# Kernel optimization log

Hardware: AMD Instinct MI355X
Metric: run time of the kernel (lower is better)

## Reference

```python
import jax, jax.numpy as jnp
import numpy as np

N_NODES = 50000
NEG_SLOPE = 0.2  # PyG GATConv default leaky_relu slope


def gat_conv(x, src, dst, W, a_src, a_dst, b):
    """One PyG-style GATConv (concat heads, add_self_loops already applied).
    x: [N, F_in]; W: [H*C, F_in]; a_src/a_dst: [H, C]; b: [H*C]."""
    N = x.shape[0]
    H, C = a_src.shape
    h = (x @ W.T).reshape(N, H, C)                       # [N,H,C]
    alpha_src = jnp.einsum('nhc,hc->nh', h, a_src)       # [N,H]
    alpha_dst = jnp.einsum('nhc,hc->nh', h, a_dst)       # [N,H]
    e = alpha_src[src] + alpha_dst[dst]                  # [E,H]
    e = jax.nn.leaky_relu(e, NEG_SLOPE)
    # segment softmax over incoming edges of each dst node, per head
    m = jax.ops.segment_max(e, dst, num_segments=N)      # [N,H]
    w = jnp.exp(e - m[dst])                              # [E,H]
    s = jax.ops.segment_sum(w, dst, num_segments=N)      # [N,H]
    alpha = w / (s[dst] + 1e-16)                         # [E,H]
    msg = alpha[:, :, None] * h[src]                     # [E,H,C]
    out = jax.ops.segment_sum(msg, dst, num_segments=N)  # [N,H,C]
    return out.reshape(N, H * C) + b


def setup_inputs() -> dict:
    key = jax.random.key(0)
    ks = jax.random.split(key, 8)
    N, E, F_in, H, C, L = N_NODES, 800000, 128, 4, 32, 3
    x = jax.random.normal(ks[0], (N, F_in), dtype=jnp.float32)
    edge_index = jax.random.randint(ks[1], (2, E), 0, N, dtype=jnp.int32)
    Ws = jax.random.normal(ks[2], (L, H * C, F_in), dtype=jnp.float32) * 0.1
    att_src = jax.random.normal(ks[3], (L, H, C), dtype=jnp.float32) * 0.1
    att_dst = jax.random.normal(ks[4], (L, H, C), dtype=jnp.float32) * 0.1
    conv_bias = jnp.zeros((L, H * C), dtype=jnp.float32)
    Wf = jax.random.normal(ks[5], (32, H * C), dtype=jnp.float32) * 0.1
    bf = jnp.zeros((32,), dtype=jnp.float32)
    return {"x": x, "Ws": Ws, "att_src": att_src, "att_dst": att_dst,
            "conv_bias": conv_bias, "Wf": Wf, "bf": bf, "edge_index": edge_index}


def reference(x, Ws, att_src, att_dst, conv_bias, Wf, bf, edge_index):
    N = x.shape[0]
    # PyG GATConv add_self_loops=True (default): append i->i for every node
    loop = jnp.arange(N, dtype=edge_index.dtype)
    src = jnp.concatenate([edge_index[0], loop])
    dst = jnp.concatenate([edge_index[1], loop])
    for l in range(Ws.shape[0]):
        x = gat_conv(x, src, dst, Ws[l], att_src[l], att_dst[l], conv_bias[l])
        x = jax.nn.relu(x)
        # F.dropout(p=0.1, training=False) is identity in eval mode
    return x @ Wf.T + bf
```

## Files before the change

kernel.cpp:

```cpp
#include <hip/hip_runtime.h>
#include <hip/hip_bf16.h>
#include <math.h>

#define N_NODES 50000
#define NE      800000
#define ETOT    (NE + N_NODES)
#define F       128
#define NHEAD   4
#define NEG     0.2f

#define SCAN_B 256
#define NBLK   ((N_NODES + SCAN_B - 1) / SCAN_B)

typedef __attribute__((ext_vector_type(8))) short bf16x8;
typedef __attribute__((ext_vector_type(4))) float f32x4;
typedef _Float16 f16x8 __attribute__((ext_vector_type(8)));


__global__ void k_deg(const int* __restrict__ ei, int* __restrict__ deg,
                      int* __restrict__ rank) {
    int i = blockIdx.x * blockDim.x + threadIdx.x;
    if (i < ETOT) {
        int d = (i < NE) ? ei[NE + i] : (i - NE);
        rank[i] = atomicAdd(&deg[d], 1);
    }
}

__global__ void k_scan1(const int* __restrict__ deg, int* __restrict__ bsum) {
    __shared__ int sm[SCAN_B];
    int i = blockIdx.x * SCAN_B + threadIdx.x;
    sm[threadIdx.x] = (i < N_NODES) ? deg[i] : 0;
    __syncthreads();
    for (int s = SCAN_B / 2; s > 0; s >>= 1) {
        if (threadIdx.x < s) sm[threadIdx.x] += sm[threadIdx.x + s];
        __syncthreads();
    }
    if (threadIdx.x == 0) bsum[blockIdx.x] = sm[0];
}

__global__ void k_scan2(int* __restrict__ bsum) {
    __shared__ int sm[SCAN_B];
    int t = threadIdx.x;
    int v = (t < NBLK) ? bsum[t] : 0;
    sm[t] = v; __syncthreads();
    for (int s = 1; s < SCAN_B; s <<= 1) {
        int a = (t >= s) ? sm[t - s] : 0;
        __syncthreads();
        sm[t] += a;
        __syncthreads();
    }
    if (t < NBLK) bsum[t] = sm[t] - v;
}

__global__ void k_scan3(const int* __restrict__ deg, const int* __restrict__ bsum,
                        int* __restrict__ rowptr) {
    __shared__ int sm[SCAN_B];
    int t = threadIdx.x;
    int i = blockIdx.x * SCAN_B + t;
    int v = (i < N_NODES) ? deg[i] : 0;
    sm[t] = v; __syncthreads();
    for (int s = 1; s < SCAN_B; s <<= 1) {
        int a = (t >= s) ? sm[t - s] : 0;
        __syncthreads();
        sm[t] += a;
        __syncthreads();
    }
    int excl = sm[t] - v + bsum[blockIdx.x];
    if (i < N_NODES) rowptr[i] = excl;
    if (i == N_NODES - 1) rowptr[N_NODES] = excl + v;
}

__global__ void k_fill(const int* __restrict__ ei, const int* __restrict__ rowptr,
                       const int* __restrict__ rank, int* __restrict__ col) {
    int i = blockIdx.x * blockDim.x + threadIdx.x;
    if (i < ETOT) {
        int s, d;
        if (i < NE) { s = ei[i]; d = ei[NE + i]; }
        else        { s = i - NE; d = s; }
        col[rowptr[d] + rank[i]] = s;
    }
}


__device__ __forceinline__ unsigned short f2bf(float x) {
    unsigned int u = __float_as_uint(x);
    u += 0x7FFFu + ((u >> 16) & 1u);
    return (unsigned short)(u >> 16);
}
__device__ __forceinline__ float bf2f(unsigned short h) {
    return __uint_as_float(((unsigned int)h) << 16);
}
__device__ __forceinline__ void cvt8(float4 a, float4 b, bf16x8* hi, bf16x8* lo) {
    float f[8] = {a.x, a.y, a.z, a.w, b.x, b.y, b.z, b.w};
    bf16x8 h, l;
#pragma unroll
    for (int j = 0; j < 8; j++) {
        unsigned short hu = f2bf(f[j]);
        h[j] = (short)hu;
        l[j] = (short)f2bf(f[j] - bf2f(hu));
    }
    *hi = h; *lo = l;
}
__device__ __forceinline__ void cvt8h(float4 a, float4 b, f16x8* hi, f16x8* lo) {
    float f[8] = {a.x, a.y, a.z, a.w, b.x, b.y, b.z, b.w};
    f16x8 h, l;
#pragma unroll
    for (int j = 0; j < 8; j++) {
        _Float16 hh = (_Float16)f[j];
        h[j] = hh;
        l[j] = (_Float16)(f[j] - (float)hh);
    }
    *hi = h; *lo = l;
}

__device__ __forceinline__ int lds_unit(int m, int q) {
    return 4 * m + (q ^ ((m >> 1) & 3));
}

#define GM 64


__global__ __launch_bounds__(256) void k_gemm(const float* __restrict__ X,
                                              const float* __restrict__ W,
                                              const float* __restrict__ a_s,
                                              const float* __restrict__ a_d,
                                              _Float16* __restrict__ hout,
                                              float* __restrict__ asrc,
                                              float* __restrict__ adst) {
    __shared__ short Ah[256 * 8], Al[256 * 8];
    __shared__ short Bh[512 * 8], Bl[512 * 8];
    int tid = threadIdx.x;
    int bm = blockIdx.x * GM;

    int am = tid >> 2, aq = tid & 3;
    int xunit = ((am >> 4) << 6) + lds_unit(am & 15, aq);
    int wj = tid >> 2, wq = tid & 3;
    int wunit = ((wj >> 4) << 6) + lds_unit(wj & 15, wq);

    int lane = tid & 63, wv = tid >> 6;
    int fm = lane & 15, fq = lane >> 4;
    int a_unit = (wv << 6) + lds_unit(fm, fq);
    int b_unit0 = lds_unit(fm, fq);

    f32x4 acc[8];
#pragma unroll
    for (int nt = 0; nt < 8; nt++) acc[nt] = (f32x4){0.f, 0.f, 0.f, 0.f};

    float4 xp0, xp1, wp0, wp1, wp2, wp3;
    int gr = bm + am;
    bool xok = (gr < N_NODES);
    const float* xrow = X + (size_t)gr * F + aq * 8;
    const float* wrow1 = W + (size_t)wj * F + wq * 8;
    const float* wrow2 = W + (size_t)(wj + 64) * F + wq * 8;
    float4 z4 = make_float4(0.f, 0.f, 0.f, 0.f);

    auto load_tile = [&](int k0) {
        xp0 = xok ? *(const float4*)(xrow + k0)     : z4;
        xp1 = xok ? *(const float4*)(xrow + k0 + 4) : z4;
        wp0 = *(const float4*)(wrow1 + k0);
        wp1 = *(const float4*)(wrow1 + k0 + 4);
        wp2 = *(const float4*)(wrow2 + k0);
        wp3 = *(const float4*)(wrow2 + k0 + 4);
    };
    auto store_tile = [&]() {
        bf16x8 hi, lo;
        cvt8(xp0, xp1, &hi, &lo);
        *(bf16x8*)&Ah[xunit * 8] = hi;  *(bf16x8*)&Al[xunit * 8] = lo;
        cvt8(wp0, wp1, &hi, &lo);
        *(bf16x8*)&Bh[wunit * 8] = hi;  *(bf16x8*)&Bl[wunit * 8] = lo;
        cvt8(wp2, wp3, &hi, &lo);
        *(bf16x8*)&Bh[(wunit + 256) * 8] = hi;  *(bf16x8*)&Bl[(wunit + 256) * 8] = lo;
    };

    load_tile(0);
    store_tile();
    __syncthreads();

#pragma unroll
    for (int t = 0; t < 4; t++) {
        if (t < 3) load_tile((t + 1) * 32);
        bf16x8 ah = *(bf16x8*)&Ah[a_unit * 8];
        bf16x8 al = *(bf16x8*)&Al[a_unit * 8];
#pragma unroll
        for (int nt = 0; nt < 8; nt++) {
            int bu = ((nt << 6) + b_unit0) * 8;
            bf16x8 bh = *(bf16x8*)&Bh[bu];
            bf16x8 bl = *(bf16x8*)&Bl[bu];
            acc[nt] = __builtin_amdgcn_mfma_f32_16x16x32_bf16(ah, bh, acc[nt], 0, 0, 0);
            acc[nt] = __builtin_amdgcn_mfma_f32_16x16x32_bf16(ah, bl, acc[nt], 0, 0, 0);
            acc[nt] = __builtin_amdgcn_mfma_f32_16x16x32_bf16(al, bh, acc[nt], 0, 0, 0);
        }
        __syncthreads();
        if (t < 3) { store_tile(); __syncthreads(); }
    }

    float as_v[8], ad_v[8];
#pragma unroll
    for (int nt = 0; nt < 8; nt++) {
        as_v[nt] = a_s[nt * 16 + fm];
        ad_v[nt] = a_d[nt * 16 + fm];
    }
#pragma unroll
    for (int r = 0; r < 4; r++) {
        int n = bm + wv * 16 + fq * 4 + r;
        bool ok = (n < N_NODES);
        if (ok) {
#pragma unroll
            for (int nt = 0; nt < 8; nt++)
                hout[(size_t)n * F + nt * 16 + fm] = (_Float16)acc[nt][r];
        }
        float ps[4], pd[4];
#pragma unroll
        for (int hh = 0; hh < 4; hh++) {
            ps[hh] = acc[2 * hh][r] * as_v[2 * hh] + acc[2 * hh + 1][r] * as_v[2 * hh + 1];
            pd[hh] = acc[2 * hh][r] * ad_v[2 * hh] + acc[2 * hh + 1][r] * ad_v[2 * hh + 1];
        }
#pragma unroll
        for (int s = 1; s < 16; s <<= 1) {
#pragma unroll
            for (int hh = 0; hh < 4; hh++) {
                ps[hh] += __shfl_xor(ps[hh], s);
                pd[hh] += __shfl_xor(pd[hh], s);
            }
        }
        if (ok && fm == 0) {
            *(float4*)&asrc[n * 4] = make_float4(ps[0], ps[1], ps[2], ps[3]);
            *(float4*)&adst[n * 4] = make_float4(pd[0], pd[1], pd[2], pd[3]);
        }
    }
}


__global__ __launch_bounds__(256) void k_gemm16(const _Float16* __restrict__ X,
                                                const float* __restrict__ W,
                                                const float* __restrict__ a_s,
                                                const float* __restrict__ a_d,
                                                _Float16* __restrict__ hout,
                                                float* __restrict__ asrc,
                                                float* __restrict__ adst) {
    __shared__ _Float16 Ahf[256 * 8];
    __shared__ _Float16 Bhf[512 * 8], Blf[512 * 8];
    int tid = threadIdx.x;
    int bm = blockIdx.x * GM;

    int am = tid >> 2, aq = tid & 3;
    int xunit = ((am >> 4) << 6) + lds_unit(am & 15, aq);
    int wj = tid >> 2, wq = tid & 3;
    int wunit = ((wj >> 4) << 6) + lds_unit(wj & 15, wq);

    int lane = tid & 63, wv = tid >> 6;
    int fm = lane & 15, fq = lane >> 4;
    int a_unit = (wv << 6) + lds_unit(fm, fq);
    int b_unit0 = lds_unit(fm, fq);

    f32x4 acc[8];
#pragma unroll
    for (int nt = 0; nt < 8; nt++) acc[nt] = (f32x4){0.f, 0.f, 0.f, 0.f};

    f16x8 xp;
    float4 wp0, wp1, wp2, wp3;
    int gr = bm + am;
    bool xok = (gr < N_NODES);
    const _Float16* xrow = X + (size_t)gr * F + aq * 8;
    const float* wrow1 = W + (size_t)wj * F + wq * 8;
    const float* wrow2 = W + (size_t)(wj + 64) * F + wq * 8;

    auto load_tile = [&](int k0) {
        f16x8 zz = {0, 0, 0, 0, 0, 0, 0, 0};
        xp = xok ? *(const f16x8*)(xrow + k0) : zz;
        wp0 = *(const float4*)(wrow1 + k0);
        wp1 = *(const float4*)(wrow1 + k0 + 4);
        wp2 = *(const float4*)(wrow2 + k0);
        wp3 = *(const float4*)(wrow2 + k0 + 4);
    };
    auto store_tile = [&]() {
        *(f16x8*)&Ahf[xunit * 8] = xp;
        f16x8 hi, lo;
        cvt8h(wp0, wp1, &hi, &lo);
        *(f16x8*)&Bhf[wunit * 8] = hi;  *(f16x8*)&Blf[wunit * 8] = lo;
        cvt8h(wp2, wp3, &hi, &lo);
        *(f16x8*)&Bhf[(wunit + 256) * 8] = hi;  *(f16x8*)&Blf[(wunit + 256) * 8] = lo;
    };

    load_tile(0);
    store_tile();
    __syncthreads();

#pragma unroll
    for (int t = 0; t < 4; t++) {
        if (t < 3) load_tile((t + 1) * 32);
        f16x8 ah = *(f16x8*)&Ahf[a_unit * 8];
#pragma unroll
        for (int nt = 0; nt < 8; nt++) {
            int bu = ((nt << 6) + b_unit0) * 8;
            f16x8 bh = *(f16x8*)&Bhf[bu];
            f16x8 bl = *(f16x8*)&Blf[bu];
            acc[nt] = __builtin_amdgcn_mfma_f32_16x16x32_f16(ah, bh, acc[nt], 0, 0, 0);
            acc[nt] = __builtin_amdgcn_mfma_f32_16x16x32_f16(ah, bl, acc[nt], 0, 0, 0);
        }
        __syncthreads();
        if (t < 3) { store_tile(); __syncthreads(); }
    }

    float as_v[8], ad_v[8];
#pragma unroll
    for (int nt = 0; nt < 8; nt++) {
        as_v[nt] = a_s[nt * 16 + fm];
        ad_v[nt] = a_d[nt * 16 + fm];
    }
#pragma unroll
    for (int r = 0; r < 4; r++) {
        int n = bm + wv * 16 + fq * 4 + r;
        bool ok = (n < N_NODES);
        if (ok) {
#pragma unroll
            for (int nt = 0; nt < 8; nt++)
                hout[(size_t)n * F + nt * 16 + fm] = (_Float16)acc[nt][r];
        }
        float ps[4], pd[4];
#pragma unroll
        for (int hh = 0; hh < 4; hh++) {
            ps[hh] = acc[2 * hh][r] * as_v[2 * hh] + acc[2 * hh + 1][r] * as_v[2 * hh + 1];
            pd[hh] = acc[2 * hh][r] * ad_v[2 * hh] + acc[2 * hh + 1][r] * ad_v[2 * hh + 1];
        }
#pragma unroll
        for (int s = 1; s < 16; s <<= 1) {
#pragma unroll
            for (int hh = 0; hh < 4; hh++) {
                ps[hh] += __shfl_xor(ps[hh], s);
                pd[hh] += __shfl_xor(pd[hh], s);
            }
        }
        if (ok && fm == 0) {
            *(float4*)&asrc[n * 4] = make_float4(ps[0], ps[1], ps[2], ps[3]);
            *(float4*)&adst[n * 4] = make_float4(pd[0], pd[1], pd[2], pd[3]);
        }
    }
}


#define EPAD 68

__global__ __launch_bounds__(256) void k_aggr(const _Float16* __restrict__ h,
                                              const float* __restrict__ asrc,
                                              const float* __restrict__ adst,
                                              const int* __restrict__ rowptr,
                                              const int* __restrict__ col,
                                              const float* __restrict__ bias,
                                              _Float16* __restrict__ xout) {
    __shared__ int   scol[4][64];
    __shared__ float swT[4][4 * EPAD];
    int wave = threadIdx.x >> 6;
    int lane = threadIdx.x & 63;
    int n = blockIdx.x * 4 + wave;
    if (n >= N_NODES) return;
    int wl = lane & 15;
    int he = lane >> 4;
    int hc = wl >> 2;
    int beg = rowptr[n], end = rowptr[n + 1];
    float4 ad4 = *(const float4*)&adst[n * 4];

    float s_run = 0.f;
    float acc[8];
#pragma unroll
    for (int j = 0; j < 8; j++) acc[j] = 0.f;

    for (int base = beg; base < end; base += 64) {
        int cnt = end - base; if (cnt > 64) cnt = 64;
        int sidx = 0;
        float4 w4 = make_float4(0.f, 0.f, 0.f, 0.f);
        if (lane < cnt) {
            sidx = col[base + lane];
            float4 av = *(const float4*)&asrc[sidx * 4];
            float ex = av.x + ad4.x, ey = av.y + ad4.y,
                  ez = av.z + ad4.z, ew = av.w + ad4.w;
            ex = (ex > 0.f) ? ex : NEG * ex;
            ey = (ey > 0.f) ? ey : NEG * ey;
            ez = (ez > 0.f) ? ez : NEG * ez;
            ew = (ew > 0.f) ? ew : NEG * ew;
            w4.x = __expf(ex); w4.y = __expf(ey);
            w4.z = __expf(ez); w4.w = __expf(ew);
        }
        scol[wave][lane] = sidx;
        swT[wave][0 * EPAD + lane] = w4.x;
        swT[wave][1 * EPAD + lane] = w4.y;
        swT[wave][2 * EPAD + lane] = w4.z;
        swT[wave][3 * EPAD + lane] = w4.w;
        __builtin_amdgcn_sched_barrier(0);
        float4 wv4 = *(float4*)&swT[wave][he * EPAD + wl * 4];
        float S = (wv4.x + wv4.y) + (wv4.z + wv4.w);
#pragma unroll
        for (int s = 1; s < 16; s <<= 1) S += __shfl_xor(S, s);
        s_run += S;
        __builtin_amdgcn_sched_barrier(0);
#pragma unroll 2
        for (int p = 0; p < cnt; p += 4) {
            int ep = p + he;
            int s = scol[wave][ep];
            float wgt = swT[wave][hc * EPAD + ep];
            f16x8 hv = *(const f16x8*)&h[(size_t)s * F + wl * 8];
#pragma unroll
            for (int j = 0; j < 8; j++)
                acc[j] = fmaf(wgt, (float)hv[j], acc[j]);
        }
        __builtin_amdgcn_sched_barrier(0);
    }

#pragma unroll
    for (int j = 0; j < 8; j++) {
        acc[j] += __shfl_xor(acc[j], 16);
        acc[j] += __shfl_xor(acc[j], 32);
    }
    float sv = __shfl(s_run, hc * 16);
    float inv = 1.f / (sv + 1e-16f);
    float4 b0 = *(const float4*)&bias[wl * 8];
    float4 b1 = *(const float4*)&bias[wl * 8 + 4];
    float bb[8] = {b0.x, b0.y, b0.z, b0.w, b1.x, b1.y, b1.z, b1.w};
    if (he == 0) {
        f16x8 st;
#pragma unroll
        for (int j = 0; j < 8; j++)
            st[j] = (_Float16)fmaxf(fmaf(acc[j], inv, bb[j]), 0.f);
        *(f16x8*)&xout[(size_t)n * F + wl * 8] = st;
    }
}


#define FCB 128

__global__ __launch_bounds__(256) void k_fc(const _Float16* __restrict__ X,
                                            const float* __restrict__ Wf,
                                            const float* __restrict__ bf,
                                            float* __restrict__ out) {
    __shared__ float WsT[128 * 36];
    __shared__ float XsT[32 * 132];
    int tid = threadIdx.x;
    int bm = blockIdx.x * FCB;

#pragma unroll
    for (int u = 0; u < 16; u++) {
        int idx = tid + 256 * u;
        int o = idx & 31, k = idx >> 5;
        WsT[k * 36 + o] = Wf[o * 128 + k];
    }

    int tx = tid & 7;
    int ty = tid >> 3;
    float acc[4][4];
#pragma unroll
    for (int i = 0; i < 4; i++)
#pragma unroll
        for (int j = 0; j < 4; j++) acc[i][j] = 0.f;

    for (int k0 = 0; k0 < 128; k0 += 32) {
        __syncthreads();
#pragma unroll
        for (int u = 0; u < 2; u++) {
            int idx = tid + 256 * u;
            int nn = idx & 127, c = idx >> 7;
            int gn = bm + nn;
            f16x8 v = {0, 0, 0, 0, 0, 0, 0, 0};
            if (gn < N_NODES) v = *(const f16x8*)&X[(size_t)gn * F + k0 + c * 8];
#pragma unroll
            for (int j = 0; j < 8; j++)
                XsT[(c * 8 + j) * 132 + nn] = (float)v[j];
        }
        __syncthreads();

#pragma unroll
        for (int kk = 0; kk < 32; kk++) {
            float4 xv = *(float4*)&XsT[kk * 132 + ty * 4];
            float4 wv = *(float4*)&WsT[(k0 + kk) * 36 + tx * 4];
            float xs[4] = {xv.x, xv.y, xv.z, xv.w};
            float ws[4] = {wv.x, wv.y, wv.z, wv.w};
#pragma unroll
            for (int i = 0; i < 4; i++)
#pragma unroll
                for (int j = 0; j < 4; j++)
                    acc[i][j] = fmaf(xs[i], ws[j], acc[i][j]);
        }
    }

    float4 bv = *(const float4*)&bf[tx * 4];
#pragma unroll
    for (int i = 0; i < 4; i++) {
        int n = bm + ty * 4 + i;
        if (n < N_NODES) {
            float4 o4 = make_float4(acc[i][0] + bv.x, acc[i][1] + bv.y,
                                    acc[i][2] + bv.z, acc[i][3] + bv.w);
            *(float4*)&out[n * 32 + tx * 4] = o4;
        }
    }
}


extern "C" void kernel_launch(void* const* d_in, const int* in_sizes, int n_in,
                              void* d_out, int out_size, void* d_ws, size_t ws_size,
                              hipStream_t stream) {
    const float* x      = (const float*)d_in[0];
    const float* Ws     = (const float*)d_in[1];
    const float* a_src  = (const float*)d_in[2];
    const float* a_dst  = (const float*)d_in[3];
    const float* cbias  = (const float*)d_in[4];
    const float* Wf     = (const float*)d_in[5];
    const float* bf     = (const float*)d_in[6];
    const int*   ei     = (const int*)d_in[7];
    float* out = (float*)d_out;

    char* p = (char*)d_ws;
    auto carve = [&](size_t bytes) {
        char* r = p;
        p += (bytes + 255) & ~(size_t)255;
        return r;
    };
    _Float16* xA   = (_Float16*)carve((size_t)N_NODES * F * 2);
    _Float16* xB   = (_Float16*)carve((size_t)N_NODES * F * 2);
    _Float16* xC   = (_Float16*)carve((size_t)N_NODES * F * 2);
    _Float16* hbuf = (_Float16*)carve((size_t)N_NODES * F * 2);
    float* asrc = (float*)carve((size_t)N_NODES * NHEAD * 4);
    float* adst = (float*)carve((size_t)N_NODES * NHEAD * 4);
    int* deg    = (int*)carve((size_t)N_NODES * 4);
    int* rowptr = (int*)carve((size_t)(N_NODES + 1) * 4);
    int* rank   = (int*)carve((size_t)ETOT * 4);
    int* bsum   = (int*)carve((size_t)SCAN_B * 4);
    int* col    = (int*)carve((size_t)ETOT * 4);

    hipMemsetAsync(deg, 0, (size_t)N_NODES * 4, stream);
    k_deg<<<(ETOT + 255) / 256, 256, 0, stream>>>(ei, deg, rank);
    k_scan1<<<NBLK, SCAN_B, 0, stream>>>(deg, bsum);
    k_scan2<<<1, SCAN_B, 0, stream>>>(bsum);
    k_scan3<<<NBLK, SCAN_B, 0, stream>>>(deg, bsum, rowptr);
    k_fill<<<(ETOT + 255) / 256, 256, 0, stream>>>(ei, rowptr, rank, col);

    int gaggr = (N_NODES + 3) / 4;
    int ggemm = (N_NODES + GM - 1) / GM;

    k_gemm<<<ggemm, 256, 0, stream>>>(x, Ws, a_src, a_dst, hbuf, asrc, adst);
    k_aggr<<<gaggr, 256, 0, stream>>>(hbuf, asrc, adst, rowptr, col, cbias, xA);

    k_gemm16<<<ggemm, 256, 0, stream>>>(xA, Ws + (size_t)F * F, a_src + F, a_dst + F,
                                        hbuf, asrc, adst);
    k_aggr<<<gaggr, 256, 0, stream>>>(hbuf, asrc, adst, rowptr, col, cbias + F, xB);

    k_gemm16<<<ggemm, 256, 0, stream>>>(xB, Ws + (size_t)2 * F * F, a_src + 2 * F,
                                        a_dst + 2 * F, hbuf, asrc, adst);
    k_aggr<<<gaggr, 256, 0, stream>>>(hbuf, asrc, adst, rowptr, col, cbias + 2 * F, xC);

    k_fc<<<(N_NODES + FCB - 1) / FCB, 256, 0, stream>>>(xC, Wf, bf, out);
}
```

Measured before the change: 323.9 us.

## Pre-split weights to fp16 hi/lo and stage GEMM tiles via global_load_lds double buffering

A new prep kernel converts the fp32 layer weights once per call into fp16 high and low parts, so the GEMMs no longer redo the split in every block. Weight tiles, and the fp16 activations in later layers, are now copied straight into LDS with global_load_lds into double buffers, which removes one barrier per K step. The first-layer GEMM moves from a bf16 three-way split to an fp16 three-way split. This adds one small kernel launch and extra workspace, drops the LDS swizzle (so bank conflicts may appear), and changes precision characteristics for layer one.

```diff
diff --git a/kernel.cpp b/kernel.cpp
--- a/kernel.cpp
+++ b/kernel.cpp
@@ -12,9 +12,14 @@
 #define SCAN_B 256
 #define NBLK   ((N_NODES + SCAN_B - 1) / SCAN_B)
 
-typedef __attribute__((ext_vector_type(8))) short bf16x8;
 typedef __attribute__((ext_vector_type(4))) float f32x4;
 typedef _Float16 f16x8 __attribute__((ext_vector_type(8)));
+
+__device__ __forceinline__ void gld16(const void* g, void* l) {
+    __builtin_amdgcn_global_load_lds(
+        (const __attribute__((address_space(1))) unsigned int*)g,
+        (__attribute__((address_space(3))) unsigned int*)l, 16, 0, 0);
+}
 
 
 __global__ void k_deg(const int* __restrict__ ei, int* __restrict__ deg,
@@ -82,118 +87,22 @@
 }
 
 
-__device__ __forceinline__ unsigned short f2bf(float x) {
-    unsigned int u = __float_as_uint(x);
-    u += 0x7FFFu + ((u >> 16) & 1u);
-    return (unsigned short)(u >> 16);
-}
-__device__ __forceinline__ float bf2f(unsigned short h) {
-    return __uint_as_float(((unsigned int)h) << 16);
-}
-__device__ __forceinline__ void cvt8(float4 a, float4 b, bf16x8* hi, bf16x8* lo) {
-    float f[8] = {a.x, a.y, a.z, a.w, b.x, b.y, b.z, b.w};
-    bf16x8 h, l;
-#pragma unroll
-    for (int j = 0; j < 8; j++) {
-        unsigned short hu = f2bf(f[j]);
-        h[j] = (short)hu;
-        l[j] = (short)f2bf(f[j] - bf2f(hu));
-    }
-    *hi = h; *lo = l;
-}
-__device__ __forceinline__ void cvt8h(float4 a, float4 b, f16x8* hi, f16x8* lo) {
-    float f[8] = {a.x, a.y, a.z, a.w, b.x, b.y, b.z, b.w};
-    f16x8 h, l;
-#pragma unroll
-    for (int j = 0; j < 8; j++) {
-        _Float16 hh = (_Float16)f[j];
-        h[j] = hh;
-        l[j] = (_Float16)(f[j] - (float)hh);
-    }
-    *hi = h; *lo = l;
-}
-
-__device__ __forceinline__ int lds_unit(int m, int q) {
-    return 4 * m + (q ^ ((m >> 1) & 3));
-}
+__global__ void k_prep(const float* __restrict__ Ws, _Float16* __restrict__ Wh,
+                       _Float16* __restrict__ Wl) {
+    int i = blockIdx.x * blockDim.x + threadIdx.x;
+    float w = Ws[i];
+    _Float16 h = (_Float16)w;
+    Wh[i] = h;
+    Wl[i] = (_Float16)(w - (float)h);
+}
+
 
 #define GM 64
 
-
-__global__ __launch_bounds__(256) void k_gemm(const float* __restrict__ X,
-                                              const float* __restrict__ W,
-                                              const float* __restrict__ a_s,
-                                              const float* __restrict__ a_d,
-                                              _Float16* __restrict__ hout,
-                                              float* __restrict__ asrc,
-                                              float* __restrict__ adst) {
-    __shared__ short Ah[256 * 8], Al[256 * 8];
-    __shared__ short Bh[512 * 8], Bl[512 * 8];
-    int tid = threadIdx.x;
-    int bm = blockIdx.x * GM;
-
-    int am = tid >> 2, aq = tid & 3;
-    int xunit = ((am >> 4) << 6) + lds_unit(am & 15, aq);
-    int wj = tid >> 2, wq = tid & 3;
-    int wunit = ((wj >> 4) << 6) + lds_unit(wj & 15, wq);
-
-    int lane = tid & 63, wv = tid >> 6;
-    int fm = lane & 15, fq = lane >> 4;
-    int a_unit = (wv << 6) + lds_unit(fm, fq);
-    int b_unit0 = lds_unit(fm, fq);
-
-    f32x4 acc[8];
-#pragma unroll
-    for (int nt = 0; nt < 8; nt++) acc[nt] = (f32x4){0.f, 0.f, 0.f, 0.f};
-
-    float4 xp0, xp1, wp0, wp1, wp2, wp3;
-    int gr = bm + am;
-    bool xok = (gr < N_NODES);
-    const float* xrow = X + (size_t)gr * F + aq * 8;
-    const float* wrow1 = W + (size_t)wj * F + wq * 8;
-    const float* wrow2 = W + (size_t)(wj + 64) * F + wq * 8;
-    float4 z4 = make_float4(0.f, 0.f, 0.f, 0.f);
-
-    auto load_tile = [&](int k0) {
-        xp0 = xok ? *(const float4*)(xrow + k0)     : z4;
-        xp1 = xok ? *(const float4*)(xrow + k0 + 4) : z4;
-        wp0 = *(const float4*)(wrow1 + k0);
-        wp1 = *(const float4*)(wrow1 + k0 + 4);
-        wp2 = *(const float4*)(wrow2 + k0);
-        wp3 = *(const float4*)(wrow2 + k0 + 4);
-    };
-    auto store_tile = [&]() {
-        bf16x8 hi, lo;
-        cvt8(xp0, xp1, &hi, &lo);
-        *(bf16x8*)&Ah[xunit * 8] = hi;  *(bf16x8*)&Al[xunit * 8] = lo;
-        cvt8(wp0, wp1, &hi, &lo);
-        *(bf16x8*)&Bh[wunit * 8] = hi;  *(bf16x8*)&Bl[wunit * 8] = lo;
-        cvt8(wp2, wp3, &hi, &lo);
-        *(bf16x8*)&Bh[(wunit + 256) * 8] = hi;  *(bf16x8*)&Bl[(wunit + 256) * 8] = lo;
-    };
-
-    load_tile(0);
-    store_tile();
-    __syncthreads();
-
-#pragma unroll
-    for (int t = 0; t < 4; t++) {
-        if (t < 3) load_tile((t + 1) * 32);
-        bf16x8 ah = *(bf16x8*)&Ah[a_unit * 8];
-        bf16x8 al = *(bf16x8*)&Al[a_unit * 8];
-#pragma unroll
-        for (int nt = 0; nt < 8; nt++) {
-            int bu = ((nt << 6) + b_unit0) * 8;
-            bf16x8 bh = *(bf16x8*)&Bh[bu];
-            bf16x8 bl = *(bf16x8*)&Bl[bu];
-            acc[nt] = __builtin_amdgcn_mfma_f32_16x16x32_bf16(ah, bh, acc[nt], 0, 0, 0);
-            acc[nt] = __builtin_amdgcn_mfma_f32_16x16x32_bf16(ah, bl, acc[nt], 0, 0, 0);
-            acc[nt] = __builtin_amdgcn_mfma_f32_16x16x32_bf16(al, bh, acc[nt], 0, 0, 0);
-        }
-        __syncthreads();
-        if (t < 3) { store_tile(); __syncthreads(); }
-    }
-
+__device__ __forceinline__ void gemm_epilogue(
+        f32x4* acc, const float* a_s, const float* a_d,
+        _Float16* hout, float* asrc, float* adst,
+        int bm, int wv, int fm, int fq) {
     float as_v[8], ad_v[8];
 #pragma unroll
     for (int nt = 0; nt < 8; nt++) {
@@ -231,111 +140,144 @@
 }
 
 
-__global__ __launch_bounds__(256) void k_gemm16(const _Float16* __restrict__ X,
-                                                const float* __restrict__ W,
+__global__ __launch_bounds__(256) void k_gemm32(const float* __restrict__ X,
+                                                const _Float16* __restrict__ Wh,
+                                                const _Float16* __restrict__ Wl,
                                                 const float* __restrict__ a_s,
                                                 const float* __restrict__ a_d,
                                                 _Float16* __restrict__ hout,
                                                 float* __restrict__ asrc,
                                                 float* __restrict__ adst) {
-    __shared__ _Float16 Ahf[256 * 8];
-    __shared__ _Float16 Bhf[512 * 8], Blf[512 * 8];
+    __shared__ _Float16 Ah[2][64 * 32], Al[2][64 * 32];
+    __shared__ _Float16 Bh[2][128 * 32], Bl[2][128 * 32];
     int tid = threadIdx.x;
+    int lane = tid & 63, wv = tid >> 6;
     int bm = blockIdx.x * GM;
 
-    int am = tid >> 2, aq = tid & 3;
-    int xunit = ((am >> 4) << 6) + lds_unit(am & 15, aq);
-    int wj = tid >> 2, wq = tid & 3;
-    int wunit = ((wj >> 4) << 6) + lds_unit(wj & 15, wq);
-
-    int lane = tid & 63, wv = tid >> 6;
+    int sr = lane >> 2, sq = lane & 3;
+    int arow = bm + wv * 16 + sr;
+    bool xok = (arow < N_NODES);
+    const float*    xg  = X  + (size_t)arow * F + sq * 8;
+    const _Float16* bh0 = Wh + (size_t)(wv * 16 + sr) * F + sq * 8;
+    const _Float16* bh1 = Wh + (size_t)(64 + wv * 16 + sr) * F + sq * 8;
+    const _Float16* bl0 = Wl + (size_t)(wv * 16 + sr) * F + sq * 8;
+    const _Float16* bl1 = Wl + (size_t)(64 + wv * 16 + sr) * F + sq * 8;
+
     int fm = lane & 15, fq = lane >> 4;
-    int a_unit = (wv << 6) + lds_unit(fm, fq);
-    int b_unit0 = lds_unit(fm, fq);
+    int aoff = ((wv * 16 + fm) * 4 + fq) * 8;
 
     f32x4 acc[8];
 #pragma unroll
     for (int nt = 0; nt < 8; nt++) acc[nt] = (f32x4){0.f, 0.f, 0.f, 0.f};
 
-    f16x8 xp;
-    float4 wp0, wp1, wp2, wp3;
-    int gr = bm + am;
-    bool xok = (gr < N_NODES);
-    const _Float16* xrow = X + (size_t)gr * F + aq * 8;
-    const float* wrow1 = W + (size_t)wj * F + wq * 8;
-    const float* wrow2 = W + (size_t)(wj + 64) * F + wq * 8;
-
-    auto load_tile = [&](int k0) {
-        f16x8 zz = {0, 0, 0, 0, 0, 0, 0, 0};
-        xp = xok ? *(const f16x8*)(xrow + k0) : zz;
-        wp0 = *(const float4*)(wrow1 + k0);
-        wp1 = *(const float4*)(wrow1 + k0 + 4);
-        wp2 = *(const float4*)(wrow2 + k0);
-        wp3 = *(const float4*)(wrow2 + k0 + 4);
+    float4 xp0, xp1;
+    float4 z4 = make_float4(0.f, 0.f, 0.f, 0.f);
+    auto xload = [&](int k0) {
+        xp0 = xok ? *(const float4*)(xg + k0)     : z4;
+        xp1 = xok ? *(const float4*)(xg + k0 + 4) : z4;
     };
-    auto store_tile = [&]() {
-        *(f16x8*)&Ahf[xunit * 8] = xp;
-        f16x8 hi, lo;
-        cvt8h(wp0, wp1, &hi, &lo);
-        *(f16x8*)&Bhf[wunit * 8] = hi;  *(f16x8*)&Blf[wunit * 8] = lo;
-        cvt8h(wp2, wp3, &hi, &lo);
-        *(f16x8*)&Bhf[(wunit + 256) * 8] = hi;  *(f16x8*)&Blf[(wunit + 256) * 8] = lo;
+    auto xstore = [&](int buf) {
+        float f[8] = {xp0.x, xp0.y, xp0.z, xp0.w, xp1.x, xp1.y, xp1.z, xp1.w};
+        f16x8 h, l;
+#pragma unroll
+        for (int j = 0; j < 8; j++) {
+            _Float16 hh = (_Float16)f[j];
+            h[j] = hh;
+            l[j] = (_Float16)(f[j] - (float)hh);
+        }
+        *(f16x8*)&Ah[buf][(size_t)(wv * 16 + sr) * 32 + sq * 8] = h;
+        *(f16x8*)&Al[buf][(size_t)(wv * 16 + sr) * 32 + sq * 8] = l;
     };
-
-    load_tile(0);
-    store_tile();
+    auto wstage = [&](int k0, int buf) {
+        gld16(bh0 + k0, &Bh[buf][wv * 512]);
+        gld16(bh1 + k0, &Bh[buf][2048 + wv * 512]);
+        gld16(bl0 + k0, &Bl[buf][wv * 512]);
+        gld16(bl1 + k0, &Bl[buf][2048 + wv * 512]);
+    };
+
+    xload(0); wstage(0, 0); xstore(0);
     __syncthreads();
 
 #pragma unroll
     for (int t = 0; t < 4; t++) {
-        if (t < 3) load_tile((t + 1) * 32);
-        f16x8 ah = *(f16x8*)&Ahf[a_unit * 8];
+        int buf = t & 1;
+        if (t < 3) { xload((t + 1) * 32); wstage((t + 1) * 32, buf ^ 1); }
+        f16x8 ah = *(f16x8*)&Ah[buf][aoff];
+        f16x8 al = *(f16x8*)&Al[buf][aoff];
 #pragma unroll
         for (int nt = 0; nt < 8; nt++) {
-            int bu = ((nt << 6) + b_unit0) * 8;
-            f16x8 bh = *(f16x8*)&Bhf[bu];
-            f16x8 bl = *(f16x8*)&Blf[bu];
+            int bo = ((nt * 16 + fm) * 4 + fq) * 8;
+            f16x8 bh = *(f16x8*)&Bh[buf][bo];
+            f16x8 bl = *(f16x8*)&Bl[buf][bo];
             acc[nt] = __builtin_amdgcn_mfma_f32_16x16x32_f16(ah, bh, acc[nt], 0, 0, 0);
             acc[nt] = __builtin_amdgcn_mfma_f32_16x16x32_f16(ah, bl, acc[nt], 0, 0, 0);
-        }
-        __syncthreads();
-        if (t < 3) { store_tile(); __syncthreads(); }
-    }
-
-    float as_v[8], ad_v[8];
-#pragma unroll
-    for (int nt = 0; nt < 8; nt++) {
-        as_v[nt] = a_s[nt * 16 + fm];
-        ad_v[nt] = a_d[nt * 16 + fm];
-    }
-#pragma unroll
-    for (int r = 0; r < 4; r++) {
-        int n = bm + wv * 16 + fq * 4 + r;
-        bool ok = (n < N_NODES);
-        if (ok) {
-#pragma unroll
-            for (int nt = 0; nt < 8; nt++)
-                hout[(size_t)n * F + nt * 16 + fm] = (_Float16)acc[nt][r];
-        }
-        float ps[4], pd[4];
-#pragma unroll
-        for (int hh = 0; hh < 4; hh++) {
-            ps[hh] = acc[2 * hh][r] * as_v[2 * hh] + acc[2 * hh + 1][r] * as_v[2 * hh + 1];
-            pd[hh] = acc[2 * hh][r] * ad_v[2 * hh] + acc[2 * hh + 1][r] * ad_v[2 * hh + 1];
-        }
-#pragma unroll
-        for (int s = 1; s < 16; s <<= 1) {
-#pragma unroll
-            for (int hh = 0; hh < 4; hh++) {
-                ps[hh] += __shfl_xor(ps[hh], s);
-                pd[hh] += __shfl_xor(pd[hh], s);
-            }
-        }
-        if (ok && fm == 0) {
-            *(float4*)&asrc[n * 4] = make_float4(ps[0], ps[1], ps[2], ps[3]);
-            *(float4*)&adst[n * 4] = make_float4(pd[0], pd[1], pd[2], pd[3]);
-        }
-    }
+            acc[nt] = __builtin_amdgcn_mfma_f32_16x16x32_f16(al, bh, acc[nt], 0, 0, 0);
+        }
+        if (t < 3) xstore(buf ^ 1);
+        __syncthreads();
+    }
+
+    gemm_epilogue(acc, a_s, a_d, hout, asrc, adst, bm, wv, fm, fq);
+}
+
+
+__global__ __launch_bounds__(256) void k_gemm16(const _Float16* __restrict__ X,
+                                                const _Float16* __restrict__ Wh,
+                                                const _Float16* __restrict__ Wl,
+                                                const float* __restrict__ a_s,
+                                                const float* __restrict__ a_d,
+                                                _Float16* __restrict__ hout,
+                                                float* __restrict__ asrc,
+                                                float* __restrict__ adst) {
+    __shared__ _Float16 Ab[2][64 * 32];
+    __shared__ _Float16 Bh[2][128 * 32], Bl[2][128 * 32];
+    int tid = threadIdx.x;
+    int lane = tid & 63, wv = tid >> 6;
+    int bm = blockIdx.x * GM;
+
+    int sr = lane >> 2, sq = lane & 3;
+    int arow = bm + wv * 16 + sr;
+    const _Float16* ag  = X  + (size_t)arow * F + sq * 8;
+    const _Float16* bh0 = Wh + (size_t)(wv * 16 + sr) * F + sq * 8;
+    const _Float16* bh1 = Wh + (size_t)(64 + wv * 16 + sr) * F + sq * 8;
+    const _Float16* bl0 = Wl + (size_t)(wv * 16 + sr) * F + sq * 8;
+    const _Float16* bl1 = Wl + (size_t)(64 + wv * 16 + sr) * F + sq * 8;
+
+    int fm = lane & 15, fq = lane >> 4;
+    int aoff = ((wv * 16 + fm) * 4 + fq) * 8;
+
+    f32x4 acc[8];
+#pragma unroll
+    for (int nt = 0; nt < 8; nt++) acc[nt] = (f32x4){0.f, 0.f, 0.f, 0.f};
+
+    auto stage = [&](int k0, int buf) {
+        gld16(ag  + k0, &Ab[buf][wv * 512]);
+        gld16(bh0 + k0, &Bh[buf][wv * 512]);
+        gld16(bh1 + k0, &Bh[buf][2048 + wv * 512]);
+        gld16(bl0 + k0, &Bl[buf][wv * 512]);
+        gld16(bl1 + k0, &Bl[buf][2048 + wv * 512]);
+    };
+
+    stage(0, 0);
+    __syncthreads();
+
+#pragma unroll
+    for (int t = 0; t < 4; t++) {
+        int buf = t & 1;
+        if (t < 3) stage((t + 1) * 32, buf ^ 1);
+        f16x8 ah = *(f16x8*)&Ab[buf][aoff];
+#pragma unroll
+        for (int nt = 0; nt < 8; nt++) {
+            int bo = ((nt * 16 + fm) * 4 + fq) * 8;
+            f16x8 bh = *(f16x8*)&Bh[buf][bo];
+            f16x8 bl = *(f16x8*)&Bl[buf][bo];
+            acc[nt] = __builtin_amdgcn_mfma_f32_16x16x32_f16(ah, bh, acc[nt], 0, 0, 0);
+            acc[nt] = __builtin_amdgcn_mfma_f32_16x16x32_f16(ah, bl, acc[nt], 0, 0, 0);
+        }
+        __syncthreads();
+    }
+
+    gemm_epilogue(acc, a_s, a_d, hout, asrc, adst, bm, wv, fm, fq);
 }
 
 
@@ -517,6 +459,8 @@
     _Float16* xB   = (_Float16*)carve((size_t)N_NODES * F * 2);
     _Float16* xC   = (_Float16*)carve((size_t)N_NODES * F * 2);
     _Float16* hbuf = (_Float16*)carve((size_t)N_NODES * F * 2);
+    _Float16* Wh   = (_Float16*)carve((size_t)3 * F * F * 2);
+    _Float16* Wl   = (_Float16*)carve((size_t)3 * F * F * 2);
     float* asrc = (float*)carve((size_t)N_NODES * NHEAD * 4);
     float* adst = (float*)carve((size_t)N_NODES * NHEAD * 4);
     int* deg    = (int*)carve((size_t)N_NODES * 4);
@@ -525,6 +469,7 @@
     int* bsum   = (int*)carve((size_t)SCAN_B * 4);
     int* col    = (int*)carve((size_t)ETOT * 4);
 
+    k_prep<<<(3 * F * F) / 256, 256, 0, stream>>>(Ws, Wh, Wl);
     hipMemsetAsync(deg, 0, (size_t)N_NODES * 4, stream);
     k_deg<<<(ETOT + 255) / 256, 256, 0, stream>>>(ei, deg, rank);
     k_scan1<<<NBLK, SCAN_B, 0, stream>>>(deg, bsum);
@@ -535,15 +480,15 @@
     int gaggr = (N_NODES + 3) / 4;
     int ggemm = (N_NODES + GM - 1) / GM;
 
-    k_gemm<<<ggemm, 256, 0, stream>>>(x, Ws, a_src, a_dst, hbuf, asrc, adst);
+    k_gemm32<<<ggemm, 256, 0, stream>>>(x, Wh, Wl, a_src, a_dst, hbuf, asrc, adst);
     k_aggr<<<gaggr, 256, 0, stream>>>(hbuf, asrc, adst, rowptr, col, cbias, xA);
 
-    k_gemm16<<<ggemm, 256, 0, stream>>>(xA, Ws + (size_t)F * F, a_src + F, a_dst + F,
-                                        hbuf, asrc, adst);
+    k_gemm16<<<ggemm, 256, 0, stream>>>(xA, Wh + (size_t)F * F, Wl + (size_t)F * F,
+                                        a_src + F, a_dst + F, hbuf, asrc, adst);
     k_aggr<<<gaggr, 256, 0, stream>>>(hbuf, asrc, adst, rowptr, col, cbias + F, xB);
 
-    k_gemm16<<<ggemm, 256, 0, stream>>>(xB, Ws + (size_t)2 * F * F, a_src + 2 * F,
-                                        a_dst + 2 * F, hbuf, asrc, adst);
+    k_gemm16<<<ggemm, 256, 0, stream>>>(xB, Wh + (size_t)2 * F * F, Wl + (size_t)2 * F * F,
+                                        a_src + 2 * F, a_dst + 2 * F, hbuf, asrc, adst);
     k_aggr<<<gaggr, 256, 0, stream>>>(hbuf, asrc, adst, rowptr, col, cbias + 2 * F, xC);
 
     k_fc<<<(N_NODES + FCB - 1) / FCB, 256, 0, stream>>>(xC, Wf, bf, out);
```

Result: no change. 329.8 us (+1.8%).
